# Optimization experiments

Hardware: AMD Instinct MI355X
Metric: run time of the kernel (lower is better)

Reference implementation:

```python
import jax, jax.numpy as jnp
import numpy as np

B, S, HH, WW = 256, 384, 12, 16
D = HH * WW          # 192, LSTM input dim
H = 100              # hidden_dim
C = 250              # output_dim (N_CLASSES)


def setup_inputs() -> dict:
    key = jax.random.key(0)
    k1, k2, k3, k4 = jax.random.split(key, 4)
    x = jax.random.normal(k1, (B, S, HH, WW), dtype=jnp.float32)
    # Glorot-ish scaling to keep the recurrence numerically tame
    W = jax.random.normal(k2, (D, 4 * H), dtype=jnp.float32) / np.sqrt(D)
    U = jax.random.normal(k3, (H, 4 * H), dtype=jnp.float32) / np.sqrt(H)
    b = jnp.zeros((4 * H,), dtype=jnp.float32)
    Wd = jax.random.normal(k4, (H, C), dtype=jnp.float32) / np.sqrt(H)
    bd = jnp.zeros((C,), dtype=jnp.float32)
    return {"x": x, "W": W, "U": U, "b": b, "Wd": Wd, "bd": bd}


def _lstm_last_hidden(x3, W, U, b):
    # x3: [B, S, D]. Keras gate order: i, f, c(g), o.
    pre = jnp.einsum('bsd,dk->sbk', x3, W) + b  # time-major [S, B, 4H]
    h0 = jnp.zeros((x3.shape[0], H), dtype=x3.dtype)
    c0 = jnp.zeros_like(h0)

    def step(carry, xt):
        h, c = carry
        z = xt + h @ U                      # [B, 4H]
        i = jax.nn.sigmoid(z[:, 0 * H:1 * H])
        f = jax.nn.sigmoid(z[:, 1 * H:2 * H])
        g = jnp.tanh(z[:, 2 * H:3 * H])
        o = jax.nn.sigmoid(z[:, 3 * H:4 * H])
        c_new = f * c + i * g
        h_new = o * jnp.tanh(c_new)
        return (h_new, c_new), None

    (hT, _), _ = jax.lax.scan(step, (h0, c0), pre)
    return hT  # [B, H] == out[:, -1, :] since return_sequences last step = final state


def reference(x, W, U, b, Wd, bd):
    b_, s_, hh_, ww_ = x.shape
    x3 = x.reshape(b_, s_, hh_ * ww_)
    hT = _lstm_last_hidden(x3, W, U, b)
    # Dropout layers are identity at inference (training=False)
    return hT @ Wd + bd  # [B, C] logits
```

## Files before the change

kernel.cpp:

```cpp
#include <hip/hip_runtime.h>
#include <cstdint>
#include <cstddef>

#define S_LEN 384
#define BATCH 256
#define DIM   192
#define HID   100
#define G4    400
#define NCLS  250

#define LOG2E  1.4426950408889634f
#define LOG2E2 2.8853900817779268f

typedef float    f32x4   __attribute__((ext_vector_type(4)));
typedef short    bf16x8  __attribute__((ext_vector_type(8)));
typedef _Float16 half2_t __attribute__((ext_vector_type(2)));
typedef _Float16 f16x4   __attribute__((ext_vector_type(4)));
typedef _Float16 f16x8   __attribute__((ext_vector_type(8)));

static __device__ __forceinline__ unsigned short f2bf(float f) {
    unsigned u = __float_as_uint(f);
    return (unsigned short)((u + 0x7FFFu + ((u >> 16) & 1u)) >> 16);
}

template<int CTRL>
static __device__ __forceinline__ float fdpp(float x) {
    return __int_as_float(
        __builtin_amdgcn_mov_dpp(__float_as_int(x), CTRL, 0xF, 0xF, true));
}
#define DPP_X1 0xB1
#define DPP_X2 0x4E
#define DPP_B0 0x00
#define DPP_B1 0x55
#define DPP_B2 0xAA
#define DPP_B3 0xFF

__global__ void prep(const float* __restrict__ W, const float* __restrict__ U,
                     unsigned short* __restrict__ Wt, half2_t* __restrict__ Ut4)
{
    int bid = blockIdx.x;
    if (bid < 300) {
        int i = bid * 256 + threadIdx.x;
        if (i >= G4 * DIM) return;
        int k = i / DIM, d = i - k * DIM;
        Wt[i] = f2bf(W[(size_t)d * G4 + k]);
    } else {
        int i = (bid - 300) * 256 + threadIdx.x;
        if (i >= 20800) return;
        int n    = i / 208;
        int rem  = i - n * 208;
        int q    = rem / 52;
        int rem2 = rem - q * 52;
        int m    = rem2 / 13;
        int r    = rem2 - m * 13;
        int col  = (q ^ m) * HID + n;
        int j0   = 26 * q + 2 * r;
        half2_t v;
        v.x = (_Float16)(j0     < HID ? U[(size_t)j0       * G4 + col] : 0.0f);
        v.y = (_Float16)(j0 + 1 < HID ? U[(size_t)(j0 + 1) * G4 + col] : 0.0f);
        Ut4[i] = v;
    }
}

__global__ __launch_bounds__(256, 2)
void gemm_pre(const float* __restrict__ x, const unsigned short* __restrict__ Wt,
              const float* __restrict__ bias, _Float16* __restrict__ preh,
              int s_start, int chunk)
{
    __shared__ unsigned int xs[64 * 100];
    __shared__ unsigned int wsh[400 * 20];

    const int t    = threadIdx.x;
    const int lane = t & 63;
    const int w    = t >> 6;
    const int nsb  = chunk >> 6;
    const int b    = blockIdx.x / nsb;
    const int sblk = blockIdx.x - b * nsb;
    const float* __restrict__ xb = x + ((size_t)b * S_LEN + s_start + sblk * 64) * DIM;

#pragma unroll
    for (int r = 0; r < 12; ++r) {
        int i = t + r * 256;
        int row = i / 48, c4 = i - row * 48;
        float4 v = ((const float4*)(xb + (size_t)row * DIM))[c4];
        xs[row * 100 + c4 * 2]     = (unsigned)f2bf(v.x) | ((unsigned)f2bf(v.y) << 16);
        xs[row * 100 + c4 * 2 + 1] = (unsigned)f2bf(v.z) | ((unsigned)f2bf(v.w) << 16);
    }

    const int m = lane & 15, q = lane >> 4;

    float bv[25];
#pragma unroll
    for (int ct = 0; ct < 25; ++ct) bv[ct] = bias[ct * 16 + m];

    f32x4 acc[25];
#pragma unroll
    for (int ct = 0; ct < 25; ++ct) acc[ct] = (f32x4){0.f, 0.f, 0.f, 0.f};

    for (int dc = 0; dc < 6; ++dc) {
        if (dc) __syncthreads();
#pragma unroll
        for (int r = 0; r < 7; ++r) {
            int i = t + r * 256;
            if (i < 1600) {
                int k = i >> 2, u4 = i & 3;
                uint4 v = *(const uint4*)(Wt + (size_t)k * DIM + dc * 32 + u4 * 8);
                *(uint4*)(wsh + k * 20 + u4 * 4) = v;
            }
        }
        __syncthreads();

        const unsigned short* xp = (const unsigned short*)xs
                                   + (16 * w + m) * 200 + dc * 32 + q * 8;
        bf16x8 af = *(const bf16x8*)xp;
#pragma unroll
        for (int ct = 0; ct < 25; ++ct) {
            const unsigned short* bp = (const unsigned short*)wsh
                                       + (ct * 16 + m) * 40 + q * 8;
            bf16x8 bf = *(const bf16x8*)bp;
            acc[ct] = __builtin_amdgcn_mfma_f32_16x16x32_bf16(af, bf, acc[ct], 0, 0, 0);
        }
    }

    _Float16* __restrict__ pb = preh + (size_t)b * G4 * chunk + (size_t)sblk * 64
                                + 16 * w + q * 4;
#pragma unroll
    for (int ct = 0; ct < 25; ++ct) {
        f16x4 v;
        v[0] = (_Float16)(acc[ct][0] + bv[ct]);
        v[1] = (_Float16)(acc[ct][1] + bv[ct]);
        v[2] = (_Float16)(acc[ct][2] + bv[ct]);
        v[3] = (_Float16)(acc[ct][3] + bv[ct]);
        *(f16x4*)(pb + (size_t)(ct * 16 + m) * chunk) = v;
    }
}

__global__ __launch_bounds__(512, 2)
void lstm_scan(const _Float16* __restrict__ preh, const half2_t* __restrict__ Ut4,
               const float* __restrict__ Wd, const float* __restrict__ bd,
               float* __restrict__ out, float* __restrict__ state,
               int nsteps, int first, int last)
{
    __shared__ __align__(16) _Float16 h2[2][4][40];
    __shared__ __align__(16) float hf32[HID];

    const int b  = blockIdx.x;
    const int t  = threadIdx.x;
    const int q  = t & 3;
    const int nr = t >> 2;
    const bool active = (nr < HID);
    const int n  = active ? nr : HID - 1;
    const int wq = n / 26, wi = n - wq * 26;

    half2_t Uc[4][13];
#pragma unroll
    for (int m = 0; m < 4; ++m) {
        const half2_t* up = Ut4 + (size_t)((n * 4 + q) * 4 + m) * 13;
#pragma unroll
        for (int r = 0; r < 13; ++r) Uc[m][r] = up[r];
    }

    if (t < 320) ((_Float16*)h2)[t] = (_Float16)0.f;
    float c;
    if (first) {
        c = 0.f;
        __syncthreads();
    } else {
        c = state[BATCH * HID + b * HID + n];
        __syncthreads();
        if (t < HID) h2[0][t / 26][t - (t / 26) * 26] = (_Float16)state[b * HID + t];
        __syncthreads();
    }

    const _Float16* __restrict__ zp = preh + ((size_t)b * G4 + q * HID + n) * nsteps;

    const float scale = (q == 2) ? -LOG2E2 : -LOG2E;
    const float Aact  = (q == 2) ? 2.0f : 1.0f;
    const float Bact  = (q == 2) ? -1.0f : 0.0f;

    float hn_last = 0.f;

    auto step = [&](float zk, int cur) {
        const _Float16* hb = &h2[cur][q][0];
        f16x8   g0 = *(const f16x8*)(hb);
        f16x8   g1 = *(const f16x8*)(hb + 8);
        f16x8   g2 = *(const f16x8*)(hb + 16);
        half2_t g3 = *(const half2_t*)(hb + 24);
        half2_t hp[13];
        hp[0]  = __builtin_shufflevector(g0, g0, 0, 1);
        hp[1]  = __builtin_shufflevector(g0, g0, 2, 3);
        hp[2]  = __builtin_shufflevector(g0, g0, 4, 5);
        hp[3]  = __builtin_shufflevector(g0, g0, 6, 7);
        hp[4]  = __builtin_shufflevector(g1, g1, 0, 1);
        hp[5]  = __builtin_shufflevector(g1, g1, 2, 3);
        hp[6]  = __builtin_shufflevector(g1, g1, 4, 5);
        hp[7]  = __builtin_shufflevector(g1, g1, 6, 7);
        hp[8]  = __builtin_shufflevector(g2, g2, 0, 1);
        hp[9]  = __builtin_shufflevector(g2, g2, 2, 3);
        hp[10] = __builtin_shufflevector(g2, g2, 4, 5);
        hp[11] = __builtin_shufflevector(g2, g2, 6, 7);
        hp[12] = g3;

        float p0 = 0.f, p1 = 0.f, p2 = 0.f, p3 = 0.f;
#pragma unroll
        for (int r = 0; r < 13; ++r) {
            p0 = __builtin_amdgcn_fdot2(Uc[0][r], hp[r], p0, false);
            p1 = __builtin_amdgcn_fdot2(Uc[1][r], hp[r], p1, false);
            p2 = __builtin_amdgcn_fdot2(Uc[2][r], hp[r], p2, false);
            p3 = __builtin_amdgcn_fdot2(Uc[3][r], hp[r], p3, false);
        }
        float s0 = p0 + fdpp<DPP_X1>(p1);
        float s2 = p2 + fdpp<DPP_X1>(p3);
        float a  = s0 + fdpp<DPP_X2>(s2) + zk;

        float v = fmaf(Aact,
                       __builtin_amdgcn_rcpf(1.0f + __builtin_amdgcn_exp2f(scale * a)),
                       Bact);

        float bi = fdpp<DPP_B0>(v);
        float bf = fdpp<DPP_B1>(v);
        float bg = fdpp<DPP_B2>(v);
        float bo = fdpp<DPP_B3>(v);

        c = fmaf(bf, c, bi * bg);
        float tc = fmaf(2.0f,
                        __builtin_amdgcn_rcpf(1.0f + __builtin_amdgcn_exp2f(-LOG2E2 * c)),
                        -1.0f);
        float hn = bo * tc;
        if (q == 0 && active) h2[cur ^ 1][wq][wi] = (_Float16)hn;
        hn_last = hn;
        __syncthreads();
    };

    f16x8 zv = *(const f16x8*)(zp);
    for (int s8 = 0; s8 < nsteps; s8 += 8) {
        f16x8 zvn = zv;
        if (s8 + 8 < nsteps) zvn = *(const f16x8*)(zp + s8 + 8);
#pragma unroll
        for (int k = 0; k < 8; ++k)
            step((float)zv[k], k & 1);
        zv = zvn;
    }

    if (last) {
        if (q == 0 && active) hf32[n] = hn_last;
        __syncthreads();
        if (t < NCLS) {
            float acc2 = bd[t];
            const float4* h4 = (const float4*)hf32;
#pragma unroll 5
            for (int j4 = 0; j4 < 25; ++j4) {
                float4 hv = h4[j4];
                acc2 = fmaf(hv.x, Wd[(size_t)(4 * j4 + 0) * NCLS + t], acc2);
                acc2 = fmaf(hv.y, Wd[(size_t)(4 * j4 + 1) * NCLS + t], acc2);
                acc2 = fmaf(hv.z, Wd[(size_t)(4 * j4 + 2) * NCLS + t], acc2);
                acc2 = fmaf(hv.w, Wd[(size_t)(4 * j4 + 3) * NCLS + t], acc2);
            }
            out[(size_t)b * NCLS + t] = acc2;
        }
    } else {
        if (q == 0 && active) {
            state[b * HID + n] = hn_last;
            state[BATCH * HID + b * HID + n] = c;
        }
    }
}

extern "C" void kernel_launch(void* const* d_in, const int* in_sizes, int n_in,
                              void* d_out, int out_size, void* d_ws, size_t ws_size,
                              hipStream_t stream)
{
    const float* x    = (const float*)d_in[0];
    const float* W    = (const float*)d_in[1];
    const float* U    = (const float*)d_in[2];
    const float* bias = (const float*)d_in[3];
    const float* Wd   = (const float*)d_in[4];
    const float* bd   = (const float*)d_in[5];
    float* out = (float*)d_out;

    const size_t fixed_dw = 51200 + 20800 + 38400;
    int chunk = 64;
    if      (ws_size >= (fixed_dw + (size_t)384 * 51200) * 4) chunk = 384;
    else if (ws_size >= (fixed_dw + (size_t)192 * 51200) * 4) chunk = 192;
    const int nchunks = S_LEN / chunk;

    unsigned int* wsb = (unsigned int*)d_ws;
    float*          state = (float*)wsb;
    half2_t*        Ut4   = (half2_t*)(wsb + 51200);
    unsigned short* Wt    = (unsigned short*)(wsb + 72000);
    _Float16*       preh  = (_Float16*)(wsb + 110400);

    prep<<<382, 256, 0, stream>>>(W, U, Wt, Ut4);

    for (int ci = 0; ci < nchunks; ++ci) {
        const int s0 = ci * chunk;
        gemm_pre<<<BATCH * (chunk >> 6), 256, 0, stream>>>(x, Wt, bias, preh, s0, chunk);
        lstm_scan<<<BATCH, 512, 0, stream>>>(preh, Ut4, Wd, bd, out, state,
                                             chunk, ci == 0 ? 1 : 0,
                                             ci == nchunks - 1 ? 1 : 0);
    }
}
```

Before: 322.8 us.

## Compute LSTM recurrent matvec with f16 MFMA instead of per-thread fdot2

Rewrites the recurrent scan so each 256-thread block computes h@U with 16x16x32 f16 MFMA instructions. The U weights are repacked in a new padded 448x128 layout and held in registers, and each wave handles two 16-column hidden tiles across all four gates. This removes the DPP cross-lane reductions and broadcasts and halves the block size. The trade-off is that each MFMA uses only one of its 16 output rows (the batch dimension is 1 per block), so most tensor-core work is wasted. Each sequential step also still pays MFMA latency plus a block barrier.

```diff
diff --git a/kernel.cpp b/kernel.cpp
--- a/kernel.cpp
+++ b/kernel.cpp
@@ -23,20 +23,15 @@
     return (unsigned short)((u + 0x7FFFu + ((u >> 16) & 1u)) >> 16);
 }
 
-template<int CTRL>
-static __device__ __forceinline__ float fdpp(float x) {
-    return __int_as_float(
-        __builtin_amdgcn_mov_dpp(__float_as_int(x), CTRL, 0xF, 0xF, true));
-}
-#define DPP_X1 0xB1
-#define DPP_X2 0x4E
-#define DPP_B0 0x00
-#define DPP_B1 0x55
-#define DPP_B2 0xAA
-#define DPP_B3 0xFF
+static __device__ __forceinline__ float sigm(float x) {
+    return __builtin_amdgcn_rcpf(1.0f + __builtin_amdgcn_exp2f(-LOG2E * x));
+}
+static __device__ __forceinline__ float tanhp(float x) {
+    return fmaf(2.0f, __builtin_amdgcn_rcpf(1.0f + __builtin_amdgcn_exp2f(-LOG2E2 * x)), -1.0f);
+}
 
 __global__ void prep(const float* __restrict__ W, const float* __restrict__ U,
-                     unsigned short* __restrict__ Wt, half2_t* __restrict__ Ut4)
+                     unsigned short* __restrict__ Wt, _Float16* __restrict__ Ub)
 {
     int bid = blockIdx.x;
     if (bid < 300) {
@@ -46,19 +41,11 @@
         Wt[i] = f2bf(W[(size_t)d * G4 + k]);
     } else {
         int i = (bid - 300) * 256 + threadIdx.x;
-        if (i >= 20800) return;
-        int n    = i / 208;
-        int rem  = i - n * 208;
-        int q    = rem / 52;
-        int rem2 = rem - q * 52;
-        int m    = rem2 / 13;
-        int r    = rem2 - m * 13;
-        int col  = (q ^ m) * HID + n;
-        int j0   = 26 * q + 2 * r;
-        half2_t v;
-        v.x = (_Float16)(j0     < HID ? U[(size_t)j0       * G4 + col] : 0.0f);
-        v.y = (_Float16)(j0 + 1 < HID ? U[(size_t)(j0 + 1) * G4 + col] : 0.0f);
-        Ut4[i] = v;
+        if (i >= 448 * 128) return;
+        int col = i >> 7, k = i & 127;
+        int g = col / 112, n = col - g * 112;
+        float v = (n < HID && k < HID) ? U[(size_t)k * G4 + g * HID + n] : 0.0f;
+        Ub[i] = (_Float16)v;
     }
 }
 
@@ -135,115 +122,141 @@
     }
 }
 
-__global__ __launch_bounds__(512, 2)
-void lstm_scan(const _Float16* __restrict__ preh, const half2_t* __restrict__ Ut4,
+#define MF4(ACC, B0, B1, B2, B3)                                              \
+    ACC = __builtin_amdgcn_mfma_f32_16x16x32_f16(A0, B0, ACC, 0, 0, 0);       \
+    ACC = __builtin_amdgcn_mfma_f32_16x16x32_f16(A1, B1, ACC, 0, 0, 0);       \
+    ACC = __builtin_amdgcn_mfma_f32_16x16x32_f16(A2, B2, ACC, 0, 0, 0);       \
+    ACC = __builtin_amdgcn_mfma_f32_16x16x32_f16(A3, B3, ACC, 0, 0, 0);
+
+#define LDU(VAR, NCOL, G, KC)                                                 \
+    VAR = *(const f16x8*)(Ub + (size_t)((G) * 112 + (NCOL)) * 128 + (KC) * 32 + q * 8);
+
+__global__ __launch_bounds__(256, 1)
+void lstm_scan(const _Float16* __restrict__ preh, const _Float16* __restrict__ Ub,
                const float* __restrict__ Wd, const float* __restrict__ bd,
                float* __restrict__ out, float* __restrict__ state,
                int nsteps, int first, int last)
 {
-    __shared__ __align__(16) _Float16 h2[2][4][40];
+    __shared__ __align__(16) _Float16 hbuf[2][128];
     __shared__ __align__(16) float hf32[HID];
 
-    const int b  = blockIdx.x;
-    const int t  = threadIdx.x;
-    const int q  = t & 3;
-    const int nr = t >> 2;
-    const bool active = (nr < HID);
-    const int n  = active ? nr : HID - 1;
-    const int wq = n / 26, wi = n - wq * 26;
-
-    half2_t Uc[4][13];
-#pragma unroll
-    for (int m = 0; m < 4; ++m) {
-        const half2_t* up = Ut4 + (size_t)((n * 4 + q) * 4 + m) * 13;
-#pragma unroll
-        for (int r = 0; r < 13; ++r) Uc[m][r] = up[r];
-    }
-
-    if (t < 320) ((_Float16*)h2)[t] = (_Float16)0.f;
-    float c;
+    const int b    = blockIdx.x;
+    const int t    = threadIdx.x;
+    const int lane = t & 63;
+    const int w    = t >> 6;
+    const int m    = lane & 15;
+    const int q    = lane >> 4;
+
+    const int j0  = w;
+    const int j1  = (w < 3) ? (w + 4) : 3;
+    const int n0  = 16 * j0 + m;
+    const int n1r = 16 * j1 + m;
+    const bool v1 = (n1r < HID);
+    const int n1  = v1 ? n1r : (HID - 1);
+
+    f16x8 U00, U01, U02, U03, U10, U11, U12, U13;
+    f16x8 U20, U21, U22, U23, U30, U31, U32, U33;
+    f16x8 V00, V01, V02, V03, V10, V11, V12, V13;
+    f16x8 V20, V21, V22, V23, V30, V31, V32, V33;
+    LDU(U00, n0, 0, 0) LDU(U01, n0, 0, 1) LDU(U02, n0, 0, 2) LDU(U03, n0, 0, 3)
+    LDU(U10, n0, 1, 0) LDU(U11, n0, 1, 1) LDU(U12, n0, 1, 2) LDU(U13, n0, 1, 3)
+    LDU(U20, n0, 2, 0) LDU(U21, n0, 2, 1) LDU(U22, n0, 2, 2) LDU(U23, n0, 2, 3)
+    LDU(U30, n0, 3, 0) LDU(U31, n0, 3, 1) LDU(U32, n0, 3, 2) LDU(U33, n0, 3, 3)
+    LDU(V00, n1r, 0, 0) LDU(V01, n1r, 0, 1) LDU(V02, n1r, 0, 2) LDU(V03, n1r, 0, 3)
+    LDU(V10, n1r, 1, 0) LDU(V11, n1r, 1, 1) LDU(V12, n1r, 1, 2) LDU(V13, n1r, 1, 3)
+    LDU(V20, n1r, 2, 0) LDU(V21, n1r, 2, 1) LDU(V22, n1r, 2, 2) LDU(V23, n1r, 2, 3)
+    LDU(V30, n1r, 3, 0) LDU(V31, n1r, 3, 1) LDU(V32, n1r, 3, 2) LDU(V33, n1r, 3, 3)
+
+    float c0, c1;
+    if (t < 128) { hbuf[0][t] = (_Float16)0.f; hbuf[1][t] = (_Float16)0.f; }
     if (first) {
-        c = 0.f;
-        __syncthreads();
+        c0 = 0.f; c1 = 0.f;
     } else {
-        c = state[BATCH * HID + b * HID + n];
-        __syncthreads();
-        if (t < HID) h2[0][t / 26][t - (t / 26) * 26] = (_Float16)state[b * HID + t];
-        __syncthreads();
-    }
-
-    const _Float16* __restrict__ zp = preh + ((size_t)b * G4 + q * HID + n) * nsteps;
-
-    const float scale = (q == 2) ? -LOG2E2 : -LOG2E;
-    const float Aact  = (q == 2) ? 2.0f : 1.0f;
-    const float Bact  = (q == 2) ? -1.0f : 0.0f;
-
-    float hn_last = 0.f;
-
-    auto step = [&](float zk, int cur) {
-        const _Float16* hb = &h2[cur][q][0];
-        f16x8   g0 = *(const f16x8*)(hb);
-        f16x8   g1 = *(const f16x8*)(hb + 8);
-        f16x8   g2 = *(const f16x8*)(hb + 16);
-        half2_t g3 = *(const half2_t*)(hb + 24);
-        half2_t hp[13];
-        hp[0]  = __builtin_shufflevector(g0, g0, 0, 1);
-        hp[1]  = __builtin_shufflevector(g0, g0, 2, 3);
-        hp[2]  = __builtin_shufflevector(g0, g0, 4, 5);
-        hp[3]  = __builtin_shufflevector(g0, g0, 6, 7);
-        hp[4]  = __builtin_shufflevector(g1, g1, 0, 1);
-        hp[5]  = __builtin_shufflevector(g1, g1, 2, 3);
-        hp[6]  = __builtin_shufflevector(g1, g1, 4, 5);
-        hp[7]  = __builtin_shufflevector(g1, g1, 6, 7);
-        hp[8]  = __builtin_shufflevector(g2, g2, 0, 1);
-        hp[9]  = __builtin_shufflevector(g2, g2, 2, 3);
-        hp[10] = __builtin_shufflevector(g2, g2, 4, 5);
-        hp[11] = __builtin_shufflevector(g2, g2, 6, 7);
-        hp[12] = g3;
-
-        float p0 = 0.f, p1 = 0.f, p2 = 0.f, p3 = 0.f;
-#pragma unroll
-        for (int r = 0; r < 13; ++r) {
-            p0 = __builtin_amdgcn_fdot2(Uc[0][r], hp[r], p0, false);
-            p1 = __builtin_amdgcn_fdot2(Uc[1][r], hp[r], p1, false);
-            p2 = __builtin_amdgcn_fdot2(Uc[2][r], hp[r], p2, false);
-            p3 = __builtin_amdgcn_fdot2(Uc[3][r], hp[r], p3, false);
-        }
-        float s0 = p0 + fdpp<DPP_X1>(p1);
-        float s2 = p2 + fdpp<DPP_X1>(p3);
-        float a  = s0 + fdpp<DPP_X2>(s2) + zk;
-
-        float v = fmaf(Aact,
-                       __builtin_amdgcn_rcpf(1.0f + __builtin_amdgcn_exp2f(scale * a)),
-                       Bact);
-
-        float bi = fdpp<DPP_B0>(v);
-        float bf = fdpp<DPP_B1>(v);
-        float bg = fdpp<DPP_B2>(v);
-        float bo = fdpp<DPP_B3>(v);
-
-        c = fmaf(bf, c, bi * bg);
-        float tc = fmaf(2.0f,
-                        __builtin_amdgcn_rcpf(1.0f + __builtin_amdgcn_exp2f(-LOG2E2 * c)),
-                        -1.0f);
-        float hn = bo * tc;
-        if (q == 0 && active) h2[cur ^ 1][wq][wi] = (_Float16)hn;
-        hn_last = hn;
-        __syncthreads();
-    };
-
-    f16x8 zv = *(const f16x8*)(zp);
-    for (int s8 = 0; s8 < nsteps; s8 += 8) {
-        f16x8 zvn = zv;
-        if (s8 + 8 < nsteps) zvn = *(const f16x8*)(zp + s8 + 8);
-#pragma unroll
-        for (int k = 0; k < 8; ++k)
-            step((float)zv[k], k & 1);
-        zv = zvn;
+        c0 = state[BATCH * HID + b * HID + n0];
+        c1 = state[BATCH * HID + b * HID + n1];
+        if (t < HID) hbuf[0][t] = (_Float16)state[b * HID + t];
+    }
+    __syncthreads();
+
+    const _Float16* __restrict__ zb = preh + (size_t)b * G4 * nsteps;
+    const int zo0 = (0 * HID + n0) * nsteps, zo1 = (1 * HID + n0) * nsteps;
+    const int zo2 = (2 * HID + n0) * nsteps, zo3 = (3 * HID + n0) * nsteps;
+    const int zo4 = (0 * HID + n1) * nsteps, zo5 = (1 * HID + n1) * nsteps;
+    const int zo6 = (2 * HID + n1) * nsteps, zo7 = (3 * HID + n1) * nsteps;
+
+    half2_t zc[8], zn[8];
+    zc[0] = *(const half2_t*)(zb + zo0); zc[1] = *(const half2_t*)(zb + zo1);
+    zc[2] = *(const half2_t*)(zb + zo2); zc[3] = *(const half2_t*)(zb + zo3);
+    zc[4] = *(const half2_t*)(zb + zo4); zc[5] = *(const half2_t*)(zb + zo5);
+    zc[6] = *(const half2_t*)(zb + zo6); zc[7] = *(const half2_t*)(zb + zo7);
+
+    float h0l = 0.f, h1l = 0.f;
+    int cur = 0;
+
+    for (int s = 0; s < nsteps; s += 2) {
+        if (s + 2 < nsteps) {
+            zn[0] = *(const half2_t*)(zb + zo0 + s + 2);
+            zn[1] = *(const half2_t*)(zb + zo1 + s + 2);
+            zn[2] = *(const half2_t*)(zb + zo2 + s + 2);
+            zn[3] = *(const half2_t*)(zb + zo3 + s + 2);
+            zn[4] = *(const half2_t*)(zb + zo4 + s + 2);
+            zn[5] = *(const half2_t*)(zb + zo5 + s + 2);
+            zn[6] = *(const half2_t*)(zb + zo6 + s + 2);
+            zn[7] = *(const half2_t*)(zb + zo7 + s + 2);
+        }
+#pragma unroll
+        for (int u = 0; u < 2; ++u) {
+            const _Float16* hb = hbuf[cur];
+            f16x8 A0 = *(const f16x8*)(hb + q * 8);
+            f16x8 A1 = *(const f16x8*)(hb + 32 + q * 8);
+            f16x8 A2 = *(const f16x8*)(hb + 64 + q * 8);
+            f16x8 A3 = *(const f16x8*)(hb + 96 + q * 8);
+
+            float zi0 = (float)zc[0][u], zf0 = (float)zc[1][u];
+            float zg0 = (float)zc[2][u], zo0f = (float)zc[3][u];
+            float zi1 = (float)zc[4][u], zf1 = (float)zc[5][u];
+            float zg1 = (float)zc[6][u], zo1f = (float)zc[7][u];
+
+            f32x4 aI0 = {zi0, zi0, zi0, zi0}, aF0 = {zf0, zf0, zf0, zf0};
+            f32x4 aG0 = {zg0, zg0, zg0, zg0}, aO0 = {zo0f, zo0f, zo0f, zo0f};
+            f32x4 aI1 = {zi1, zi1, zi1, zi1}, aF1 = {zf1, zf1, zf1, zf1};
+            f32x4 aG1 = {zg1, zg1, zg1, zg1}, aO1 = {zo1f, zo1f, zo1f, zo1f};
+
+            MF4(aI0, U00, U01, U02, U03)
+            MF4(aF0, U10, U11, U12, U13)
+            MF4(aG0, U20, U21, U22, U23)
+            MF4(aO0, U30, U31, U32, U33)
+            MF4(aI1, V00, V01, V02, V03)
+            MF4(aF1, V10, V11, V12, V13)
+            MF4(aG1, V20, V21, V22, V23)
+            MF4(aO1, V30, V31, V32, V33)
+
+            float i0 = sigm(aI0[0]), f0 = sigm(aF0[0]);
+            float g0 = tanhp(aG0[0]), o0 = sigm(aO0[0]);
+            c0  = fmaf(f0, c0, i0 * g0);
+            h0l = o0 * tanhp(c0);
+
+            float i1 = sigm(aI1[0]), f1 = sigm(aF1[0]);
+            float g1 = tanhp(aG1[0]), o1 = sigm(aO1[0]);
+            c1  = fmaf(f1, c1, i1 * g1);
+            h1l = o1 * tanhp(c1);
+
+            if (q == 0) {
+                hbuf[cur ^ 1][n0] = (_Float16)h0l;
+                if (v1) hbuf[cur ^ 1][n1r] = (_Float16)h1l;
+            }
+            __syncthreads();
+            cur ^= 1;
+        }
+#pragma unroll
+        for (int r = 0; r < 8; ++r) zc[r] = zn[r];
     }
 
     if (last) {
-        if (q == 0 && active) hf32[n] = hn_last;
+        if (q == 0) {
+            hf32[n0] = h0l;
+            if (v1) hf32[n1r] = h1l;
+        }
         __syncthreads();
         if (t < NCLS) {
             float acc2 = bd[t];
@@ -259,9 +272,13 @@
             out[(size_t)b * NCLS + t] = acc2;
         }
     } else {
-        if (q == 0 && active) {
-            state[b * HID + n] = hn_last;
-            state[BATCH * HID + b * HID + n] = c;
+        if (q == 0) {
+            state[b * HID + n0] = h0l;
+            state[BATCH * HID + b * HID + n0] = c0;
+            if (v1) {
+                state[b * HID + n1r] = h1l;
+                state[BATCH * HID + b * HID + n1r] = c1;
+            }
         }
     }
 }
@@ -278,7 +295,7 @@
     const float* bd   = (const float*)d_in[5];
     float* out = (float*)d_out;
 
-    const size_t fixed_dw = 51200 + 20800 + 38400;
+    const size_t fixed_dw = 51200 + 28672 + 38400;
     int chunk = 64;
     if      (ws_size >= (fixed_dw + (size_t)384 * 51200) * 4) chunk = 384;
     else if (ws_size >= (fixed_dw + (size_t)192 * 51200) * 4) chunk = 192;
@@ -286,16 +303,16 @@
 
     unsigned int* wsb = (unsigned int*)d_ws;
     float*          state = (float*)wsb;
-    half2_t*        Ut4   = (half2_t*)(wsb + 51200);
-    unsigned short* Wt    = (unsigned short*)(wsb + 72000);
-    _Float16*       preh  = (_Float16*)(wsb + 110400);
-
-    prep<<<382, 256, 0, stream>>>(W, U, Wt, Ut4);
+    _Float16*       Ub    = (_Float16*)(wsb + 51200);
+    unsigned short* Wt    = (unsigned short*)(wsb + 79872);
+    _Float16*       preh  = (_Float16*)(wsb + 118272);
+
+    prep<<<524, 256, 0, stream>>>(W, U, Wt, Ub);
 
     for (int ci = 0; ci < nchunks; ++ci) {
         const int s0 = ci * chunk;
         gemm_pre<<<BATCH * (chunk >> 6), 256, 0, stream>>>(x, Wt, bias, preh, s0, chunk);
-        lstm_scan<<<BATCH, 512, 0, stream>>>(preh, Ut4, Wd, bd, out, state,
+        lstm_scan<<<BATCH, 256, 0, stream>>>(preh, Ub, Wd, bd, out, state,
                                              chunk, ci == 0 ? 1 : 0,
                                              ci == nchunks - 1 ? 1 : 0);
     }
```

Result: slower. 526.6 us (+63.2%).

## Fuse input projection GEMM into LSTM scan with double-buffered LDS windows

Applied to the files above, without the earlier changes.

Removes the separate gemm_pre kernel and the fp16 pre-activation buffer in global memory. The scan kernel now computes the x·W projection for the next 16-step window with MFMA into a double-buffered LDS buffer, interleaved with the recurrence on the current window. It also prefetches x two windows ahead. W is prearranged into an MFMA fragment layout in prep, and the chunked state save and restore path is dropped. The cost is extra register and LDS pressure in the latency-bound scan kernel, and MFMA work that may lengthen each window's serial step chain.

```diff
diff --git a/kernel.cpp b/kernel.cpp
--- a/kernel.cpp
+++ b/kernel.cpp
@@ -9,6 +9,11 @@
 #define G4    400
 #define NCLS  250
 
+#define WSTEPS 16
+#define NWIN   24
+#define NTILES 28
+#define NKC    6
+
 #define LOG2E  1.4426950408889634f
 #define LOG2E2 2.8853900817779268f
 
@@ -21,6 +26,12 @@
 static __device__ __forceinline__ unsigned short f2bf(float f) {
     unsigned u = __float_as_uint(f);
     return (unsigned short)((u + 0x7FFFu + ((u >> 16) & 1u)) >> 16);
+}
+
+static __device__ __forceinline__ unsigned cvtpk(float a, float b) {
+    unsigned r;
+    asm("v_cvt_pk_bf16_f32 %0, %1, %2" : "=v"(r) : "v"(a), "v"(b));
+    return r;
 }
 
 template<int CTRL>
@@ -36,24 +47,32 @@
 #define DPP_B3 0xFF
 
 __global__ void prep(const float* __restrict__ W, const float* __restrict__ U,
-                     unsigned short* __restrict__ Wt, half2_t* __restrict__ Ut4)
+                     unsigned short* __restrict__ Wf, half2_t* __restrict__ Ut4)
 {
     int bid = blockIdx.x;
-    if (bid < 300) {
+    if (bid < 336) {
         int i = bid * 256 + threadIdx.x;
-        if (i >= G4 * DIM) return;
-        int k = i / DIM, d = i - k * DIM;
-        Wt[i] = f2bf(W[(size_t)d * G4 + k]);
+        int e    = i & 7;
+        int fi   = i >> 3;
+        int lane = fi & 63;
+        int ck   = fi >> 6;
+        int ct   = ck / 6, kc = ck - ct * 6;
+        int m    = lane & 15, q = lane >> 4;
+        int gate = ct / 7, jj = ct - gate * 7;
+        int unit = jj * 16 + m;
+        int d    = kc * 32 + q * 8 + e;
+        float v  = (unit < HID) ? W[(size_t)d * G4 + gate * HID + unit] : 0.0f;
+        Wf[i] = f2bf(v);
     } else {
-        int i = (bid - 300) * 256 + threadIdx.x;
+        int i = (bid - 336) * 256 + threadIdx.x;
         if (i >= 20800) return;
         int n    = i / 208;
         int rem  = i - n * 208;
         int q    = rem / 52;
         int rem2 = rem - q * 52;
-        int m    = rem2 / 13;
-        int r    = rem2 - m * 13;
-        int col  = (q ^ m) * HID + n;
+        int mm   = rem2 / 13;
+        int r    = rem2 - mm * 13;
+        int col  = (q ^ mm) * HID + n;
         int j0   = 26 * q + 2 * r;
         half2_t v;
         v.x = (_Float16)(j0     < HID ? U[(size_t)j0       * G4 + col] : 0.0f);
@@ -62,117 +81,96 @@
     }
 }
 
-__global__ __launch_bounds__(256, 2)
-void gemm_pre(const float* __restrict__ x, const unsigned short* __restrict__ Wt,
-              const float* __restrict__ bias, _Float16* __restrict__ preh,
-              int s_start, int chunk)
-{
-    __shared__ unsigned int xs[64 * 100];
-    __shared__ unsigned int wsh[400 * 20];
-
-    const int t    = threadIdx.x;
-    const int lane = t & 63;
-    const int w    = t >> 6;
-    const int nsb  = chunk >> 6;
-    const int b    = blockIdx.x / nsb;
-    const int sblk = blockIdx.x - b * nsb;
-    const float* __restrict__ xb = x + ((size_t)b * S_LEN + s_start + sblk * 64) * DIM;
-
-#pragma unroll
-    for (int r = 0; r < 12; ++r) {
-        int i = t + r * 256;
-        int row = i / 48, c4 = i - row * 48;
-        float4 v = ((const float4*)(xb + (size_t)row * DIM))[c4];
-        xs[row * 100 + c4 * 2]     = (unsigned)f2bf(v.x) | ((unsigned)f2bf(v.y) << 16);
-        xs[row * 100 + c4 * 2 + 1] = (unsigned)f2bf(v.z) | ((unsigned)f2bf(v.w) << 16);
-    }
-
-    const int m = lane & 15, q = lane >> 4;
-
-    float bv[25];
-#pragma unroll
-    for (int ct = 0; ct < 25; ++ct) bv[ct] = bias[ct * 16 + m];
-
-    f32x4 acc[25];
-#pragma unroll
-    for (int ct = 0; ct < 25; ++ct) acc[ct] = (f32x4){0.f, 0.f, 0.f, 0.f};
-
-    for (int dc = 0; dc < 6; ++dc) {
-        if (dc) __syncthreads();
-#pragma unroll
-        for (int r = 0; r < 7; ++r) {
-            int i = t + r * 256;
-            if (i < 1600) {
-                int k = i >> 2, u4 = i & 3;
-                uint4 v = *(const uint4*)(Wt + (size_t)k * DIM + dc * 32 + u4 * 8);
-                *(uint4*)(wsh + k * 20 + u4 * 4) = v;
-            }
-        }
-        __syncthreads();
-
-        const unsigned short* xp = (const unsigned short*)xs
-                                   + (16 * w + m) * 200 + dc * 32 + q * 8;
-        bf16x8 af = *(const bf16x8*)xp;
-#pragma unroll
-        for (int ct = 0; ct < 25; ++ct) {
-            const unsigned short* bp = (const unsigned short*)wsh
-                                       + (ct * 16 + m) * 40 + q * 8;
-            bf16x8 bf = *(const bf16x8*)bp;
-            acc[ct] = __builtin_amdgcn_mfma_f32_16x16x32_bf16(af, bf, acc[ct], 0, 0, 0);
-        }
-    }
-
-    _Float16* __restrict__ pb = preh + (size_t)b * G4 * chunk + (size_t)sblk * 64
-                                + 16 * w + q * 4;
-#pragma unroll
-    for (int ct = 0; ct < 25; ++ct) {
-        f16x4 v;
-        v[0] = (_Float16)(acc[ct][0] + bv[ct]);
-        v[1] = (_Float16)(acc[ct][1] + bv[ct]);
-        v[2] = (_Float16)(acc[ct][2] + bv[ct]);
-        v[3] = (_Float16)(acc[ct][3] + bv[ct]);
-        *(f16x4*)(pb + (size_t)(ct * 16 + m) * chunk) = v;
-    }
-}
-
-__global__ __launch_bounds__(512, 2)
-void lstm_scan(const _Float16* __restrict__ preh, const half2_t* __restrict__ Ut4,
-               const float* __restrict__ Wd, const float* __restrict__ bd,
-               float* __restrict__ out, float* __restrict__ state,
-               int nsteps, int first, int last)
+__global__ __launch_bounds__(512)
+__attribute__((amdgpu_waves_per_eu(2, 2)))
+void scan_fused(const float* __restrict__ x, const unsigned short* __restrict__ Wf,
+                const half2_t* __restrict__ Ut4, const float* __restrict__ bias,
+                const float* __restrict__ Wd, const float* __restrict__ bd,
+                float* __restrict__ out)
 {
     __shared__ __align__(16) _Float16 h2[2][4][40];
     __shared__ __align__(16) float hf32[HID];
+    __shared__ __align__(16) _Float16 zbuf[2][448 * WSTEPS];
 
     const int b  = blockIdx.x;
     const int t  = threadIdx.x;
+
     const int q  = t & 3;
     const int nr = t >> 2;
     const bool active = (nr < HID);
     const int n  = active ? nr : HID - 1;
     const int wq = n / 26, wi = n - wq * 26;
 
+    const int lane = t & 63;
+    const int w    = t >> 6;
+    const int m    = lane & 15;
+    const int q4   = lane >> 4;
+    const int ntile = (w < 4) ? 4 : 3;
+    const int tbase = (w < 4) ? (w * 4) : (16 + (w - 4) * 3);
+
+    float bv[4];
+#pragma unroll
+    for (int i = 0; i < 4; ++i) {
+        int ct   = tbase + i;
+        int gate = ct / 7, jj = ct - gate * 7;
+        int unit = jj * 16 + m;
+        bv[i] = (i < ntile && unit < HID) ? bias[gate * HID + unit] : 0.0f;
+    }
+
+    const float* __restrict__ xb = x + (size_t)b * S_LEN * DIM;
+    float4 xv[NKC][2];
+
+#define LOADX(S0)                                                             \
+    { int xr = (S0) + m;                                                      \
+      _Pragma("unroll")                                                       \
+      for (int kc = 0; kc < NKC; ++kc) {                                      \
+          const float* p = xb + (size_t)xr * DIM + kc * 32 + q4 * 8;          \
+          xv[kc][0] = *(const float4*)p;                                      \
+          xv[kc][1] = *(const float4*)(p + 4);                                \
+      } }
+
+#define PRODUCE(NB)                                                           \
+    { bf16x8 Af[NKC];                                                         \
+      _Pragma("unroll")                                                       \
+      for (int kc = 0; kc < NKC; ++kc) {                                      \
+          int4 ai;                                                            \
+          ai.x = (int)cvtpk(xv[kc][0].x, xv[kc][0].y);                        \
+          ai.y = (int)cvtpk(xv[kc][0].z, xv[kc][0].w);                        \
+          ai.z = (int)cvtpk(xv[kc][1].x, xv[kc][1].y);                        \
+          ai.w = (int)cvtpk(xv[kc][1].z, xv[kc][1].w);                        \
+          Af[kc] = *(bf16x8*)&ai;                                             \
+      }                                                                       \
+      _Pragma("unroll")                                                       \
+      for (int i = 0; i < 4; ++i) if (i < ntile) {                            \
+          int ct = tbase + i;                                                 \
+          const unsigned short* bp = Wf + ((size_t)ct * NKC * 64 + lane) * 8; \
+          f32x4 acc = {bv[i], bv[i], bv[i], bv[i]};                           \
+          _Pragma("unroll")                                                   \
+          for (int kc = 0; kc < NKC; ++kc) {                                  \
+              bf16x8 Bf = *(const bf16x8*)(bp + (size_t)kc * 512);            \
+              acc = __builtin_amdgcn_mfma_f32_16x16x32_bf16(Af[kc], Bf, acc, 0, 0, 0); \
+          }                                                                   \
+          f16x4 zq;                                                           \
+          zq[0] = (_Float16)acc[0]; zq[1] = (_Float16)acc[1];                 \
+          zq[2] = (_Float16)acc[2]; zq[3] = (_Float16)acc[3];                 \
+          *(f16x4*)&zbuf[NB][(ct * 16 + m) * WSTEPS + q4 * 4] = zq;           \
+      } }
+
     half2_t Uc[4][13];
 #pragma unroll
-    for (int m = 0; m < 4; ++m) {
-        const half2_t* up = Ut4 + (size_t)((n * 4 + q) * 4 + m) * 13;
-#pragma unroll
-        for (int r = 0; r < 13; ++r) Uc[m][r] = up[r];
+    for (int mm = 0; mm < 4; ++mm) {
+        const half2_t* up = Ut4 + (size_t)((n * 4 + q) * 4 + mm) * 13;
+#pragma unroll
+        for (int r = 0; r < 13; ++r) Uc[mm][r] = up[r];
     }
 
     if (t < 320) ((_Float16*)h2)[t] = (_Float16)0.f;
-    float c;
-    if (first) {
-        c = 0.f;
-        __syncthreads();
-    } else {
-        c = state[BATCH * HID + b * HID + n];
-        __syncthreads();
-        if (t < HID) h2[0][t / 26][t - (t / 26) * 26] = (_Float16)state[b * HID + t];
-        __syncthreads();
-    }
-
-    const _Float16* __restrict__ zp = preh + ((size_t)b * G4 + q * HID + n) * nsteps;
+    float c = 0.f;
+
+    LOADX(0);
+    PRODUCE(0);
+    LOADX(WSTEPS);
+    __syncthreads();
 
     const float scale = (q == 2) ? -LOG2E2 : -LOG2E;
     const float Aact  = (q == 2) ? 2.0f : 1.0f;
@@ -232,37 +230,33 @@
         __syncthreads();
     };
 
-    f16x8 zv = *(const f16x8*)(zp);
-    for (int s8 = 0; s8 < nsteps; s8 += 8) {
-        f16x8 zvn = zv;
-        if (s8 + 8 < nsteps) zvn = *(const f16x8*)(zp + s8 + 8);
-#pragma unroll
-        for (int k = 0; k < 8; ++k)
-            step((float)zv[k], k & 1);
-        zv = zvn;
-    }
-
-    if (last) {
-        if (q == 0 && active) hf32[n] = hn_last;
-        __syncthreads();
-        if (t < NCLS) {
-            float acc2 = bd[t];
-            const float4* h4 = (const float4*)hf32;
+    const int col = q * 112 + n;
+
+    for (int j = 0; j < NWIN; ++j) {
+        f16x8 zA = *(const f16x8*)&zbuf[j & 1][col * WSTEPS];
+        f16x8 zB = *(const f16x8*)&zbuf[j & 1][col * WSTEPS + 8];
+        if (j < NWIN - 1) PRODUCE((j + 1) & 1);
+        if (j < NWIN - 2) LOADX((j + 2) * WSTEPS);
+#pragma unroll
+        for (int k = 0; k < 8; ++k) step((float)zA[k], k & 1);
+#pragma unroll
+        for (int k = 0; k < 8; ++k) step((float)zB[k], k & 1);
+    }
+
+    if (q == 0 && active) hf32[n] = hn_last;
+    __syncthreads();
+    if (t < NCLS) {
+        float acc2 = bd[t];
+        const float4* h4 = (const float4*)hf32;
 #pragma unroll 5
-            for (int j4 = 0; j4 < 25; ++j4) {
-                float4 hv = h4[j4];
-                acc2 = fmaf(hv.x, Wd[(size_t)(4 * j4 + 0) * NCLS + t], acc2);
-                acc2 = fmaf(hv.y, Wd[(size_t)(4 * j4 + 1) * NCLS + t], acc2);
-                acc2 = fmaf(hv.z, Wd[(size_t)(4 * j4 + 2) * NCLS + t], acc2);
-                acc2 = fmaf(hv.w, Wd[(size_t)(4 * j4 + 3) * NCLS + t], acc2);
-            }
-            out[(size_t)b * NCLS + t] = acc2;
+        for (int j4 = 0; j4 < 25; ++j4) {
+            float4 hv = h4[j4];
+            acc2 = fmaf(hv.x, Wd[(size_t)(4 * j4 + 0) * NCLS + t], acc2);
+            acc2 = fmaf(hv.y, Wd[(size_t)(4 * j4 + 1) * NCLS + t], acc2);
+            acc2 = fmaf(hv.z, Wd[(size_t)(4 * j4 + 2) * NCLS + t], acc2);
+            acc2 = fmaf(hv.w, Wd[(size_t)(4 * j4 + 3) * NCLS + t], acc2);
         }
-    } else {
-        if (q == 0 && active) {
-            state[b * HID + n] = hn_last;
-            state[BATCH * HID + b * HID + n] = c;
-        }
+        out[(size_t)b * NCLS + t] = acc2;
     }
 }
 
@@ -278,25 +272,10 @@
     const float* bd   = (const float*)d_in[5];
     float* out = (float*)d_out;
 
-    const size_t fixed_dw = 51200 + 20800 + 38400;
-    int chunk = 64;
-    if      (ws_size >= (fixed_dw + (size_t)384 * 51200) * 4) chunk = 384;
-    else if (ws_size >= (fixed_dw + (size_t)192 * 51200) * 4) chunk = 192;
-    const int nchunks = S_LEN / chunk;
-
     unsigned int* wsb = (unsigned int*)d_ws;
-    float*          state = (float*)wsb;
-    half2_t*        Ut4   = (half2_t*)(wsb + 51200);
-    unsigned short* Wt    = (unsigned short*)(wsb + 72000);
-    _Float16*       preh  = (_Float16*)(wsb + 110400);
-
-    prep<<<382, 256, 0, stream>>>(W, U, Wt, Ut4);
-
-    for (int ci = 0; ci < nchunks; ++ci) {
-        const int s0 = ci * chunk;
-        gemm_pre<<<BATCH * (chunk >> 6), 256, 0, stream>>>(x, Wt, bias, preh, s0, chunk);
-        lstm_scan<<<BATCH, 512, 0, stream>>>(preh, Ut4, Wd, bd, out, state,
-                                             chunk, ci == 0 ? 1 : 0,
-                                             ci == nchunks - 1 ? 1 : 0);
-    }
-}
+    unsigned short* Wf  = (unsigned short*)wsb;
+    half2_t*        Ut4 = (half2_t*)(wsb + 43008);
+
+    prep<<<418, 256, 0, stream>>>(W, U, Wf, Ut4);
+    scan_fused<<<BATCH, 512, 0, stream>>>(x, Wf, Ut4, bias, Wd, bd, out);
+}
```

New measurement: 314.2 us. -2.6%, faster.
